# Optimization experiments

Measured on AMD Instinct MI355X. Metric: run time of the kernel, lower is better.

The kernel has to match this reference:

```python
import jax, jax.numpy as jnp
import numpy as np

G, S, M = 4, 2048, 1024   # groups (batch), tokens per group, emb dim
E, H, K = 8, 4096, 2      # experts, mlp dim, top-k
CAP = int(K * S / E * 1.25)  # expert capacity = 640
AUX_COEF, Z_COEF = 0.01, 0.001


def setup_inputs() -> dict:
    key = jax.random.key(0)
    k1, k2, k3, k4, k5 = jax.random.split(key, 5)
    return {
        "inputs": jax.random.normal(k1, (G, S, M), jnp.float32),
        "paddings": jnp.zeros((G, S), jnp.float32),  # 1.0 = padded token
        "router_w": jax.random.normal(k2, (M, E), jnp.float32) / np.sqrt(M),
        "wi_gate": jax.random.normal(k3, (E, M, H), jnp.float32) / np.sqrt(M),
        "wi_0": jax.random.normal(k4, (E, M, H), jnp.float32) / np.sqrt(M),
        "wo": jax.random.normal(k5, (E, H, M), jnp.float32) / np.sqrt(H),
    }


def reference(inputs, paddings, router_w, wi_gate, wi_0, wo):
    # Router
    logits = jnp.einsum('gsm,me->gse', inputs, router_w)          # [G,S,E]
    probs = jax.nn.softmax(logits, axis=-1)
    top_p, top_i = jax.lax.top_k(probs, K)                        # [G,S,K]

    nonpad = 1.0 - paddings                                       # [G,S]
    exp_mask = jax.nn.one_hot(top_i, E, dtype=jnp.float32)        # [G,S,K,E]
    exp_mask = exp_mask * nonpad[:, :, None, None]

    # Position in expert (capacity-limited), priority by token order then k slot
    mask_flat = exp_mask.reshape(G, S * K, E)
    pos = jnp.cumsum(mask_flat, axis=1) * mask_flat               # 1-indexed where assigned
    keep = mask_flat * (pos <= CAP)
    pos_oh = jax.nn.one_hot((pos - 1.0).astype(jnp.int32), CAP, dtype=jnp.float32)  # [G,SK,E,CAP]
    dispatch_k = (keep[..., None] * pos_oh).reshape(G, S, K, E, CAP)
    dispatch = dispatch_k.sum(axis=2)                             # [G,S,E,CAP]
    combine = jnp.einsum('gsk,gskec->gsec', top_p, dispatch_k)    # [G,S,E,CAP]

    # Dispatch -> gated expert FFN -> combine
    expert_in = jnp.einsum('gsec,gsm->egcm', dispatch, inputs)    # [E,G,CAP,M]
    h = jax.nn.silu(jnp.einsum('egcm,emh->egch', expert_in, wi_gate)) \
        * jnp.einsum('egcm,emh->egch', expert_in, wi_0)           # [E,G,CAP,H]
    expert_out = jnp.einsum('egch,ehm->egcm', h, wo)              # [E,G,CAP,M]
    output = jnp.einsum('gsec,egcm->gsm', combine, expert_out)    # [G,S,M]

    # Aux losses: load-balancing (Switch style) + router z-loss
    em = jnp.max(jax.nn.one_hot(top_i, E, dtype=jnp.float32), axis=-2)       # [G,S,E]
    lb = jnp.mean(jnp.mean(em, axis=-2) * jnp.mean(probs, axis=-2)) * E * E
    z = jnp.mean(jax.nn.logsumexp(logits, axis=-1) ** 2)
    aux_loss = AUX_COEF * lb + Z_COEF * z
    return output, aux_loss
```

## Files before the change

### kernel.cpp

```cpp
#include <hip/hip_runtime.h>
#include <hip/hip_bf16.h>
#include <math.h>

#define G 4
#define S 2048
#define MDIM 1024
#define E 8
#define HDIM 4096
#define TOPK 2
#define CAP 640
#define GC (G*CAP)

typedef __attribute__((ext_vector_type(8))) short bf16x8;
typedef __attribute__((ext_vector_type(4))) short s16x4;
typedef __attribute__((ext_vector_type(4))) float f32x4;
typedef unsigned int u32;
typedef unsigned short u16;

#define MFMA16(a,b,c) __builtin_amdgcn_mfma_f32_16x16x32_bf16(a,b,c,0,0,0)

__device__ __forceinline__ u16 f2bf(float f) {
    union { float f; u32 u; } v; v.f = f;
    u32 r = v.u + 0x7fffu + ((v.u >> 16) & 1u);
    return (u16)(r >> 16);
}

__device__ __forceinline__ void gload16(const char* gp, char* lp) {
    __builtin_amdgcn_global_load_lds((const __attribute__((address_space(1))) u32*)gp,
                                     (__attribute__((address_space(3))) u32*)lp,
                                     16, 0, 0);
}

__device__ __forceinline__ int swzb(int r) { return ((r >> 1) & 3) << 4; }

__global__ __launch_bounds__(256) void transpose_cvt(const float* __restrict__ in,
                                                     u16* __restrict__ out, int R, int C) {
    int e = blockIdx.z;
    const float* ine = in + (size_t)e * R * C;
    u16* oute = out + (size_t)e * R * C;
    __shared__ float tile[64][68];
    int t = threadIdx.x;
    int x0 = blockIdx.x * 64, y0 = blockIdx.y * 64;
    int lx = (t & 15) * 4, ly = t >> 4;
    #pragma unroll
    for (int i = 0; i < 4; ++i) {
        f32x4 v = *(const f32x4*)(ine + (size_t)(y0 + ly + i * 16) * C + x0 + lx);
        *(f32x4*)&tile[ly + i * 16][lx] = v;
    }
    __syncthreads();
    int rr0 = (t & 15) * 4, cb = t >> 4;
    #pragma unroll
    for (int p = 0; p < 4; ++p) {
        int cc = cb + p * 16;
        s16x4 pk;
        #pragma unroll
        for (int j = 0; j < 4; ++j) pk[j] = (short)f2bf(tile[rr0 + j][cc]);
        *(s16x4*)(oute + (size_t)(x0 + cc) * R + y0 + rr0) = pk;
    }
}

__global__ __launch_bounds__(256) void router_kernel(const float* __restrict__ inp,
                                                     const float* __restrict__ rw,
                                                     int* __restrict__ top_i,
                                                     float* __restrict__ top_p,
                                                     float* __restrict__ partials) {
    int wid = threadIdx.x >> 6, lane = threadIdx.x & 63;
    int tok = blockIdx.x * 4 + wid;
    const float* x = inp + (size_t)tok * MDIM;
    float acc[E] = {0.f,0.f,0.f,0.f,0.f,0.f,0.f,0.f};
    #pragma unroll
    for (int rep = 0; rep < 4; ++rep) {
        int m0 = rep * 256 + lane * 4;
        f32x4 xv = *(const f32x4*)(x + m0);
        #pragma unroll
        for (int j = 0; j < 4; ++j) {
            const float* r = rw + (size_t)(m0 + j) * E;
            float xj = xv[j];
            #pragma unroll
            for (int e = 0; e < E; ++e) acc[e] += xj * r[e];
        }
    }
    #pragma unroll
    for (int e = 0; e < E; ++e)
        #pragma unroll
        for (int off = 32; off; off >>= 1) acc[e] += __shfl_down(acc[e], off);

    __shared__ float part[4][17];
    if (lane == 0) {
        float mx = acc[0];
        #pragma unroll
        for (int e = 1; e < E; ++e) mx = fmaxf(mx, acc[e]);
        float p[E], sum = 0.f;
        #pragma unroll
        for (int e = 0; e < E; ++e) { p[e] = expf(acc[e] - mx); sum += p[e]; }
        float inv = 1.f / sum;
        #pragma unroll
        for (int e = 0; e < E; ++e) p[e] *= inv;
        float lse = logf(sum) + mx;
        int i0 = 0;
        #pragma unroll
        for (int e = 1; e < E; ++e) if (acc[e] > acc[i0]) i0 = e;
        int i1 = (i0 == 0) ? 1 : 0;
        #pragma unroll
        for (int e = 0; e < E; ++e) if (e != i0 && acc[e] > acc[i1]) i1 = e;
        top_i[tok*2+0] = i0; top_i[tok*2+1] = i1;
        top_p[tok*2+0] = p[i0]; top_p[tok*2+1] = p[i1];
        #pragma unroll
        for (int e = 0; e < E; ++e) { part[wid][e] = p[e]; part[wid][8+e] = 0.f; }
        part[wid][8+i0] = 1.f; part[wid][8+i1] = 1.f;
        part[wid][16] = lse * lse;
    }
    __syncthreads();
    if (threadIdx.x < 17) {
        float v = part[0][threadIdx.x] + part[1][threadIdx.x] +
                  part[2][threadIdx.x] + part[3][threadIdx.x];
        partials[(size_t)blockIdx.x * 17 + threadIdx.x] = v;
    }
}

__global__ __launch_bounds__(256) void reduce_partials(const float* __restrict__ partials,
                                                       float* __restrict__ sums) {
    int g = blockIdx.x, t = threadIdx.x;
    float loc[17];
    #pragma unroll
    for (int c = 0; c < 17; ++c) loc[c] = 0.f;
    for (int r = t; r < 1024; r += 256) {
        const float* pr = partials + ((size_t)g * 1024 + r) * 17;
        #pragma unroll
        for (int c = 0; c < 17; ++c) loc[c] += pr[c];
    }
    __shared__ float red[256];
    for (int c = 0; c < 17; ++c) {
        red[t] = loc[c]; __syncthreads();
        for (int off = 128; off; off >>= 1) {
            if (t < off) red[t] += red[t + off];
            __syncthreads();
        }
        if (t == 0) sums[g * 17 + c] = red[0];
        __syncthreads();
    }
}

__global__ void aux_final(const float* __restrict__ sums, float* __restrict__ out) {
    float lb = 0.f, z = 0.f;
    for (int g = 0; g < G; ++g) {
        for (int e = 0; e < E; ++e)
            lb += (sums[g*17 + 8 + e] / (float)S) * (sums[g*17 + e] / (float)S);
        z += sums[g*17 + 16];
    }
    lb = lb / (float)(G * E) * (float)(E * E);
    z /= (float)(G * S);
    out[(size_t)G * S * MDIM] = 0.01f * lb + 0.001f * z;
}

__global__ __launch_bounds__(256) void scan_kernel(const int* __restrict__ top_i,
                                                   const float* __restrict__ pad,
                                                   int* __restrict__ slot_token,
                                                   int* __restrict__ token_c) {
    int b = blockIdx.x; int g = b >> 3, e = b & 7;
    int t = threadIdx.x;
    __shared__ int sums[256];
    int base = t * 16;
    int run = 0; unsigned mask16 = 0; int loc[16];
    #pragma unroll
    for (int j = 0; j < 16; ++j) {
        int i = base + j; int s = i >> 1, k = i & 1;
        int ex = top_i[((size_t)(g * S + s)) * 2 + k];
        int m = (ex == e) && (pad[g * S + s] == 0.f);
        run += m; loc[j] = run; mask16 |= ((unsigned)m << j);
    }
    sums[t] = run; __syncthreads();
    for (int off = 1; off < 256; off <<= 1) {
        int v = (t >= off) ? sums[t - off] : 0;
        __syncthreads();
        sums[t] += v;
        __syncthreads();
    }
    int excl = sums[t] - run;
    #pragma unroll
    for (int j = 0; j < 16; ++j) {
        if ((mask16 >> j) & 1u) {
            int pos = excl + loc[j];
            if (pos <= CAP) {
                int i = base + j; int s = i >> 1, k = i & 1;
                slot_token[((size_t)(e * G + g)) * CAP + (pos - 1)] = s;
                token_c[((size_t)(g * S + s)) * 2 + k] = pos - 1;
            }
        }
    }
}

__global__ __launch_bounds__(128) void gather_kernel(const float* __restrict__ inp,
                                                     const int* __restrict__ slot_token,
                                                     u16* __restrict__ X) {
    int row = blockIdx.x;
    int t = threadIdx.x;
    int s = slot_token[row];
    int g = (row % GC) / CAP;
    bf16x8 v;
    if (s >= 0) {
        const float* src = inp + ((size_t)(g * S + s)) * MDIM + t * 8;
        f32x4 a = *(const f32x4*)src;
        f32x4 b = *(const f32x4*)(src + 4);
        #pragma unroll
        for (int j = 0; j < 4; ++j) { v[j] = (short)f2bf(a[j]); v[4+j] = (short)f2bf(b[j]); }
    } else {
        #pragma unroll
        for (int j = 0; j < 8; ++j) v[j] = 0;
    }
    *(bf16x8*)(X + (size_t)row * MDIM + t * 8) = v;
}

__global__ __launch_bounds__(512, 1) void gemm_ffn12_v5(
        const u16* __restrict__ Xb, const u16* __restrict__ WgT,
        const u16* __restrict__ W0T, u16* __restrict__ Hb) {
    extern __shared__ char smem[];
    const int NK = MDIM / 32;
    int bid = blockIdx.x;
    int swz = (bid & 7) * 320 + (bid >> 3);
    int mt = swz % 10, nt = (swz / 10) & 31, e = swz / 320;
    const char* A  = (const char*)(Xb  + (size_t)e * GC * MDIM   + (size_t)mt * 256 * MDIM);
    const char* Bg = (const char*)(WgT + (size_t)e * HDIM * MDIM + (size_t)nt * 128 * MDIM);
    const char* B0 = (const char*)(W0T + (size_t)e * HDIM * MDIM + (size_t)nt * 128 * MDIM);
    int tid = threadIdx.x, w = tid >> 6, l = tid & 63;
    int wm = w >> 2, wn = w & 3;
    int rl = l >> 2, cch = (l & 3) * 16;
    int fr = l & 15, fg = l >> 4;
    int lswz = ((fr >> 1) & 3) << 4;

    int rA0 = (0 * 8 + w) * 16 + rl, rA1 = (1 * 8 + w) * 16 + rl, rB = w * 16 + rl;
    const char* gA0 = A  + (size_t)rA0 * MDIM * 2 + (cch ^ swzb(rA0));
    const char* gA1 = A  + (size_t)rA1 * MDIM * 2 + (cch ^ swzb(rA1));
    const char* gBg = Bg + (size_t)rB  * MDIM * 2 + (cch ^ swzb(rB));
    const char* gB0 = B0 + (size_t)rB  * MDIM * 2 + (cch ^ swzb(rB));
    int baseA = (wm * 128 + fr) * 64 + ((fg * 16) ^ lswz);
    int baseB = (wn * 32  + fr) * 64 + ((fg * 16) ^ lswz);

    f32x4 ag[8][2], ao[8][2];
    #pragma unroll
    for (int i = 0; i < 8; ++i) {
        ag[i][0] = (f32x4){0,0,0,0}; ag[i][1] = (f32x4){0,0,0,0};
        ao[i][0] = (f32x4){0,0,0,0}; ao[i][1] = (f32x4){0,0,0,0};
    }

    auto stage = [&](int tt) {
        int kk = tt * 64, b = tt & 3;
        gload16(gA0 + kk, smem + b * 16384 + (0 * 8 + w) * 1024);
        gload16(gA1 + kk, smem + b * 16384 + (1 * 8 + w) * 1024);
        gload16(gBg + kk, smem + 65536 + b * 8192 + w * 1024);
        gload16(gB0 + kk, smem + 98304 + b * 8192 + w * 1024);
    };

    bf16x8 afL0[4], afL1[4];

    stage(0); stage(1);
    asm volatile("s_waitcnt vmcnt(4)" ::: "memory");
    __builtin_amdgcn_s_barrier();
    __builtin_amdgcn_sched_barrier(0);
    {
        const char* p0 = smem + baseA;
        #pragma unroll
        for (int i = 0; i < 4; ++i) afL0[i] = *(const bf16x8*)(p0 + i * 1024);
    }

    auto body = [&](int t, bf16x8 (&loC)[4], bf16x8 (&loN)[4]) {
        if (t + 2 < NK) {
            stage(t + 2);
            asm volatile("s_waitcnt vmcnt(4)" ::: "memory");
        } else {
            asm volatile("s_waitcnt vmcnt(0)" ::: "memory");
        }
        __builtin_amdgcn_s_barrier();
        __builtin_amdgcn_sched_barrier(0);
        const char* pG = smem + 65536 + (t & 3) * 8192 + baseB;
        const char* pO = smem + 98304 + (t & 3) * 8192 + baseB;
        bf16x8 bgf[2], bof[2], hi[4];
        bgf[0] = *(const bf16x8*)(pG);  bgf[1] = *(const bf16x8*)(pG + 1024);
        bof[0] = *(const bf16x8*)(pO);  bof[1] = *(const bf16x8*)(pO + 1024);
        const char* bufA = smem + (t & 3) * 16384 + baseA;
        #pragma unroll
        for (int i = 0; i < 4; ++i) hi[i] = *(const bf16x8*)(bufA + (4 + i) * 1024);
        if (t + 1 < NK) {
            const char* bufN = smem + ((t + 1) & 3) * 16384 + baseA;
            #pragma unroll
            for (int i = 0; i < 4; ++i) loN[i] = *(const bf16x8*)(bufN + i * 1024);
        }
        __builtin_amdgcn_s_setprio(1);
        #pragma unroll
        for (int fm = 0; fm < 4; ++fm)
            #pragma unroll
            for (int fn = 0; fn < 2; ++fn) {
                ag[fm][fn] = MFMA16(bgf[fn], loC[fm], ag[fm][fn]);
                ao[fm][fn] = MFMA16(bof[fn], loC[fm], ao[fm][fn]);
            }
        #pragma unroll
        for (int fm = 0; fm < 4; ++fm)
            #pragma unroll
            for (int fn = 0; fn < 2; ++fn) {
                ag[4+fm][fn] = MFMA16(bgf[fn], hi[fm], ag[4+fm][fn]);
                ao[4+fm][fn] = MFMA16(bof[fn], hi[fm], ao[4+fm][fn]);
            }
        __builtin_amdgcn_s_setprio(0);
    };

    #pragma unroll 1
    for (int t = 0; t < NK; t += 2) {
        body(t, afL0, afL1);
        body(t + 1, afL1, afL0);
    }

    u16* He = Hb + (size_t)e * GC * HDIM;
    int row0 = mt * 256 + wm * 128 + fr;
    int col0 = nt * 128 + wn * 32 + fg * 4;
    #pragma unroll
    for (int fm = 0; fm < 8; ++fm)
        #pragma unroll
        for (int fn = 0; fn < 2; ++fn) {
            s16x4 pk;
            #pragma unroll
            for (int r = 0; r < 4; ++r) {
                float gv = ag[fm][fn][r], ov = ao[fm][fn][r];
                float hv = gv / (1.f + __expf(-gv)) * ov;
                pk[r] = (short)f2bf(hv);
            }
            *(s16x4*)(He + (size_t)(row0 + fm * 16) * HDIM + col0 + fn * 16) = pk;
        }
}

__global__ __launch_bounds__(512, 1) void gemm_out_v4(
        const u16* __restrict__ Hb, const u16* __restrict__ WoT,
        float* __restrict__ EO) {
    extern __shared__ char smem[];
    const int NK = HDIM / 32;
    int bid = blockIdx.x;
    int swz = (bid & 7) * 80 + (bid >> 3);
    int nt = swz & 3, mt = (swz / 4) % 20, e = swz / 80;
    const char* A = (const char*)(Hb  + (size_t)e * GC * HDIM   + (size_t)mt * 128 * HDIM);
    const char* B = (const char*)(WoT + (size_t)e * MDIM * HDIM + (size_t)nt * 256 * HDIM);
    int tid = threadIdx.x, w = tid >> 6, l = tid & 63;
    int wm = w >> 2, wn = w & 3;
    int rl = l >> 2, cch = (l & 3) * 16;
    int fr = l & 15, fg = l >> 4;
    int lswz = ((fr >> 1) & 3) << 4;

    int rA = w * 16 + rl, rB0 = (0 * 8 + w) * 16 + rl, rB1 = (1 * 8 + w) * 16 + rl;
    const char* gA  = A + (size_t)rA  * HDIM * 2 + (cch ^ swzb(rA));
    const char* gBa = B + (size_t)rB0 * HDIM * 2 + (cch ^ swzb(rB0));
    const char* gBb = B + (size_t)rB1 * HDIM * 2 + (cch ^ swzb(rB1));
    int baseA = (wm * 64 + fr) * 64 + ((fg * 16) ^ lswz);
    int baseB = (wn * 64 + fr) * 64 + ((fg * 16) ^ lswz);

    f32x4 acc[4][4];
    #pragma unroll
    for (int i = 0; i < 4; ++i)
        #pragma unroll
        for (int j = 0; j < 4; ++j) acc[i][j] = (f32x4){0,0,0,0};

    auto stage = [&](int tt) {
        int kk = tt * 64, b = tt & 3;
        gload16(gA  + kk, smem + b * 8192 + w * 1024);
        gload16(gBa + kk, smem + 32768 + b * 16384 + (0 * 8 + w) * 1024);
        gload16(gBb + kk, smem + 32768 + b * 16384 + (1 * 8 + w) * 1024);
    };

    bf16x8 afA[4], bfA[4], afB[4], bfB[4];

    stage(0); stage(1);
    asm volatile("s_waitcnt vmcnt(3)" ::: "memory");
    __builtin_amdgcn_s_barrier();
    __builtin_amdgcn_sched_barrier(0);
    {
        const char* pA = smem + baseA;
        const char* pB = smem + 32768 + baseB;
        #pragma unroll
        for (int i = 0; i < 4; ++i) {
            afA[i] = *(const bf16x8*)(pA + i * 1024);
            bfA[i] = *(const bf16x8*)(pB + i * 1024);
        }
    }

    auto body = [&](int t, bf16x8 (&afc)[4], bf16x8 (&bfc)[4],
                    bf16x8 (&afn)[4], bf16x8 (&bfn)[4]) {
        if (t + 2 < NK) {
            stage(t + 2);
            asm volatile("s_waitcnt vmcnt(3)" ::: "memory");
        } else {
            asm volatile("s_waitcnt vmcnt(0)" ::: "memory");
        }
        __builtin_amdgcn_s_barrier();
        __builtin_amdgcn_sched_barrier(0);
        if (t + 1 < NK) {
            const char* pA = smem + ((t + 1) & 3) * 8192 + baseA;
            const char* pB = smem + 32768 + ((t + 1) & 3) * 16384 + baseB;
            #pragma unroll
            for (int i = 0; i < 4; ++i) {
                afn[i] = *(const bf16x8*)(pA + i * 1024);
                bfn[i] = *(const bf16x8*)(pB + i * 1024);
            }
        }
        __builtin_amdgcn_s_setprio(1);
        #pragma unroll
        for (int fm = 0; fm < 4; ++fm)
            #pragma unroll
            for (int fn = 0; fn < 4; ++fn)
                acc[fm][fn] = MFMA16(bfc[fn], afc[fm], acc[fm][fn]);
        __builtin_amdgcn_s_setprio(0);
    };

    #pragma unroll 1
    for (int t = 0; t < NK; t += 2) {
        body(t, afA, bfA, afB, bfB);
        body(t + 1, afB, bfB, afA, bfA);
    }

    float* Ee = EO + (size_t)e * GC * MDIM;
    int row0 = mt * 128 + wm * 64 + fr;
    int col0 = nt * 256 + wn * 64 + fg * 4;
    #pragma unroll
    for (int fm = 0; fm < 4; ++fm)
        #pragma unroll
        for (int fn = 0; fn < 4; ++fn)
            *(f32x4*)(Ee + (size_t)(row0 + fm * 16) * MDIM + col0 + fn * 16) = acc[fm][fn];
}

__global__ __launch_bounds__(256) void combine_kernel(const float* __restrict__ EO,
                                                      const int* __restrict__ top_i,
                                                      const float* __restrict__ top_p,
                                                      const int* __restrict__ token_c,
                                                      float* __restrict__ out) {
    int tok = blockIdx.x, t = threadIdx.x;
    int g = tok >> 11;
    f32x4 acc = {0.f, 0.f, 0.f, 0.f};
    #pragma unroll
    for (int k = 0; k < 2; ++k) {
        int c = token_c[tok * 2 + k];
        if (c >= 0) {
            int e = top_i[tok * 2 + k];
            float p = top_p[tok * 2 + k];
            const float* src = EO + ((size_t)e * GC + g * CAP + c) * MDIM + t * 4;
            f32x4 v = *(const f32x4*)src;
            #pragma unroll
            for (int j = 0; j < 4; ++j) acc[j] += p * v[j];
        }
    }
    *(f32x4*)(out + (size_t)tok * MDIM + t * 4) = acc;
}

extern "C" void kernel_launch(void* const* d_in, const int* in_sizes, int n_in,
                              void* d_out, int out_size, void* d_ws, size_t ws_size,
                              hipStream_t stream) {
    (void)in_sizes; (void)n_in; (void)out_size; (void)ws_size;
    const float* inputs   = (const float*)d_in[0];
    const float* paddings = (const float*)d_in[1];
    const float* router_w = (const float*)d_in[2];
    const float* wi_gate  = (const float*)d_in[3];
    const float* wi_0     = (const float*)d_in[4];
    const float* wo       = (const float*)d_in[5];
    float* out = (float*)d_out;

    char* p = (char*)d_ws;
    u16* WgT = (u16*)p; p += (size_t)E * HDIM * MDIM * 2;
    u16* W0T = (u16*)p; p += (size_t)E * HDIM * MDIM * 2;
    u16* WoT = (u16*)p; p += (size_t)E * HDIM * MDIM * 2;
    u16* Xb  = (u16*)p; p += (size_t)E * GC * MDIM * 2;
    u16* Hb  = (u16*)p; p += (size_t)E * GC * HDIM * 2;
    float* EO = (float*)p; p += (size_t)E * GC * MDIM * 4;
    int*   top_i = (int*)p;   p += (size_t)G * S * TOPK * 4;
    float* top_p = (float*)p; p += (size_t)G * S * TOPK * 4;
    int*   token_c = (int*)p; p += (size_t)G * S * TOPK * 4;
    int*   slot_token = (int*)p; p += (size_t)E * G * CAP * 4;
    float* partials = (float*)p; p += (size_t)4096 * 17 * 4;
    float* sums = (float*)p; p += 4 * 17 * 4;

    hipMemsetAsync(token_c, 0xFF, (size_t)G * S * TOPK * 4, stream);
    hipMemsetAsync(slot_token, 0xFF, (size_t)E * G * CAP * 4, stream);

    hipFuncSetAttribute((const void*)gemm_ffn12_v5,
                        hipFuncAttributeMaxDynamicSharedMemorySize, 131072);
    hipFuncSetAttribute((const void*)gemm_out_v4,
                        hipFuncAttributeMaxDynamicSharedMemorySize, 98304);

    transpose_cvt<<<dim3(HDIM/64, MDIM/64, E), 256, 0, stream>>>(wi_gate, WgT, MDIM, HDIM);
    transpose_cvt<<<dim3(HDIM/64, MDIM/64, E), 256, 0, stream>>>(wi_0,   W0T, MDIM, HDIM);
    transpose_cvt<<<dim3(MDIM/64, HDIM/64, E), 256, 0, stream>>>(wo,     WoT, HDIM, MDIM);

    router_kernel<<<G * S / 4, 256, 0, stream>>>(inputs, router_w, top_i, top_p, partials);
    reduce_partials<<<G, 256, 0, stream>>>(partials, sums);
    scan_kernel<<<G * E, 256, 0, stream>>>(top_i, paddings, slot_token, token_c);
    gather_kernel<<<E * GC, 128, 0, stream>>>(inputs, slot_token, Xb);
    gemm_ffn12_v5<<<2560, 512, 131072, stream>>>(Xb, WgT, W0T, Hb);
    gemm_out_v4<<<640, 512, 98304, stream>>>(Hb, WoT, EO);
    combine_kernel<<<G * S, 256, 0, stream>>>(EO, top_i, top_p, token_c, out);
    aux_final<<<1, 1, 0, stream>>>(sums, out);
}
```

Baseline: 796.8 us.

## Restructure expert GEMMs to 4-wave blocks with 2 blocks per CU

Both expert GEMM kernels move from 8-wave, single-block-per-CU designs with 4-stage LDS pipelines and register prefetch to 4-wave blocks with a simple double-buffered LDS pipeline and 48KB shared memory, allowing two blocks per CU. The FFN12 kernel shrinks its M tile from 256 to 128 rows, doubling its grid. The output GEMM gives each wave a larger 64x128 accumulator tile. The intent is better latency hiding through occupancy rather than deep software pipelining. The cost is a full vmcnt(0) wait plus barrier every K step and larger per-wave register footprints.

```diff
diff --git a/kernel.cpp b/kernel.cpp
--- a/kernel.cpp
+++ b/kernel.cpp
@@ -211,111 +211,85 @@
     *(bf16x8*)(X + (size_t)row * MDIM + t * 8) = v;
 }
 
-__global__ __launch_bounds__(512, 1) void gemm_ffn12_v5(
+__global__ __launch_bounds__(256, 2) void gemm_ffn12_v6(
         const u16* __restrict__ Xb, const u16* __restrict__ WgT,
         const u16* __restrict__ W0T, u16* __restrict__ Hb) {
     extern __shared__ char smem[];
     const int NK = MDIM / 32;
     int bid = blockIdx.x;
-    int swz = (bid & 7) * 320 + (bid >> 3);
-    int mt = swz % 10, nt = (swz / 10) & 31, e = swz / 320;
-    const char* A  = (const char*)(Xb  + (size_t)e * GC * MDIM   + (size_t)mt * 256 * MDIM);
+    int swz = (bid & 7) * 640 + (bid >> 3);
+    int mt = swz % 20, nt = (swz / 20) % 32, e = swz / 640;
+    const char* A  = (const char*)(Xb  + (size_t)e * GC * MDIM   + (size_t)mt * 128 * MDIM);
     const char* Bg = (const char*)(WgT + (size_t)e * HDIM * MDIM + (size_t)nt * 128 * MDIM);
     const char* B0 = (const char*)(W0T + (size_t)e * HDIM * MDIM + (size_t)nt * 128 * MDIM);
     int tid = threadIdx.x, w = tid >> 6, l = tid & 63;
-    int wm = w >> 2, wn = w & 3;
+    int wm = w >> 1, wn = w & 1;
     int rl = l >> 2, cch = (l & 3) * 16;
     int fr = l & 15, fg = l >> 4;
     int lswz = ((fr >> 1) & 3) << 4;
 
-    int rA0 = (0 * 8 + w) * 16 + rl, rA1 = (1 * 8 + w) * 16 + rl, rB = w * 16 + rl;
-    const char* gA0 = A  + (size_t)rA0 * MDIM * 2 + (cch ^ swzb(rA0));
-    const char* gA1 = A  + (size_t)rA1 * MDIM * 2 + (cch ^ swzb(rA1));
-    const char* gBg = Bg + (size_t)rB  * MDIM * 2 + (cch ^ swzb(rB));
-    const char* gB0 = B0 + (size_t)rB  * MDIM * 2 + (cch ^ swzb(rB));
-    int baseA = (wm * 128 + fr) * 64 + ((fg * 16) ^ lswz);
-    int baseB = (wn * 32  + fr) * 64 + ((fg * 16) ^ lswz);
-
-    f32x4 ag[8][2], ao[8][2];
-    #pragma unroll
-    for (int i = 0; i < 8; ++i) {
-        ag[i][0] = (f32x4){0,0,0,0}; ag[i][1] = (f32x4){0,0,0,0};
-        ao[i][0] = (f32x4){0,0,0,0}; ao[i][1] = (f32x4){0,0,0,0};
-    }
+    int r0 = 0 * 64 + w * 16 + rl, r1 = 1 * 64 + w * 16 + rl;
+    const char* gA0 = A  + (size_t)r0 * MDIM * 2 + (cch ^ swzb(r0));
+    const char* gA1 = A  + (size_t)r1 * MDIM * 2 + (cch ^ swzb(r1));
+    const char* gG0 = Bg + (size_t)r0 * MDIM * 2 + (cch ^ swzb(r0));
+    const char* gG1 = Bg + (size_t)r1 * MDIM * 2 + (cch ^ swzb(r1));
+    const char* gO0 = B0 + (size_t)r0 * MDIM * 2 + (cch ^ swzb(r0));
+    const char* gO1 = B0 + (size_t)r1 * MDIM * 2 + (cch ^ swzb(r1));
+    int baseA = (wm * 64 + fr) * 64 + ((fg * 16) ^ lswz);
+    int baseB = (wn * 64 + fr) * 64 + ((fg * 16) ^ lswz);
+
+    f32x4 ag[4][4], ao[4][4];
+    #pragma unroll
+    for (int i = 0; i < 4; ++i)
+        #pragma unroll
+        for (int j = 0; j < 4; ++j) { ag[i][j] = (f32x4){0,0,0,0}; ao[i][j] = (f32x4){0,0,0,0}; }
 
     auto stage = [&](int tt) {
-        int kk = tt * 64, b = tt & 3;
-        gload16(gA0 + kk, smem + b * 16384 + (0 * 8 + w) * 1024);
-        gload16(gA1 + kk, smem + b * 16384 + (1 * 8 + w) * 1024);
-        gload16(gBg + kk, smem + 65536 + b * 8192 + w * 1024);
-        gload16(gB0 + kk, smem + 98304 + b * 8192 + w * 1024);
+        int kk = tt * 64;
+        char* dst = smem + (tt & 1) * 24576;
+        gload16(gA0 + kk, dst + 0 * 4096 + w * 1024);
+        gload16(gA1 + kk, dst + 1 * 4096 + w * 1024);
+        gload16(gG0 + kk, dst + 8192 + 0 * 4096 + w * 1024);
+        gload16(gG1 + kk, dst + 8192 + 1 * 4096 + w * 1024);
+        gload16(gO0 + kk, dst + 16384 + 0 * 4096 + w * 1024);
+        gload16(gO1 + kk, dst + 16384 + 1 * 4096 + w * 1024);
     };
 
-    bf16x8 afL0[4], afL1[4];
-
-    stage(0); stage(1);
-    asm volatile("s_waitcnt vmcnt(4)" ::: "memory");
+    stage(0);
+    asm volatile("s_waitcnt vmcnt(0)" ::: "memory");
     __builtin_amdgcn_s_barrier();
-    __builtin_amdgcn_sched_barrier(0);
-    {
-        const char* p0 = smem + baseA;
-        #pragma unroll
-        for (int i = 0; i < 4; ++i) afL0[i] = *(const bf16x8*)(p0 + i * 1024);
-    }
-
-    auto body = [&](int t, bf16x8 (&loC)[4], bf16x8 (&loN)[4]) {
-        if (t + 2 < NK) {
-            stage(t + 2);
-            asm volatile("s_waitcnt vmcnt(4)" ::: "memory");
-        } else {
-            asm volatile("s_waitcnt vmcnt(0)" ::: "memory");
-        }
-        __builtin_amdgcn_s_barrier();
-        __builtin_amdgcn_sched_barrier(0);
-        const char* pG = smem + 65536 + (t & 3) * 8192 + baseB;
-        const char* pO = smem + 98304 + (t & 3) * 8192 + baseB;
-        bf16x8 bgf[2], bof[2], hi[4];
-        bgf[0] = *(const bf16x8*)(pG);  bgf[1] = *(const bf16x8*)(pG + 1024);
-        bof[0] = *(const bf16x8*)(pO);  bof[1] = *(const bf16x8*)(pO + 1024);
-        const char* bufA = smem + (t & 3) * 16384 + baseA;
-        #pragma unroll
-        for (int i = 0; i < 4; ++i) hi[i] = *(const bf16x8*)(bufA + (4 + i) * 1024);
-        if (t + 1 < NK) {
-            const char* bufN = smem + ((t + 1) & 3) * 16384 + baseA;
-            #pragma unroll
-            for (int i = 0; i < 4; ++i) loN[i] = *(const bf16x8*)(bufN + i * 1024);
-        }
+
+    #pragma unroll 1
+    for (int t = 0; t < NK; ++t) {
+        if (t + 1 < NK) stage(t + 1);
+        const char* bufc = smem + (t & 1) * 24576;
+        bf16x8 af[4], bg_[4], bo_[4];
+        #pragma unroll
+        for (int fm = 0; fm < 4; ++fm) af[fm]  = *(const bf16x8*)(bufc + baseA + fm * 1024);
+        #pragma unroll
+        for (int fn = 0; fn < 4; ++fn) bg_[fn] = *(const bf16x8*)(bufc + 8192  + baseB + fn * 1024);
+        #pragma unroll
+        for (int fn = 0; fn < 4; ++fn) bo_[fn] = *(const bf16x8*)(bufc + 16384 + baseB + fn * 1024);
         __builtin_amdgcn_s_setprio(1);
         #pragma unroll
         for (int fm = 0; fm < 4; ++fm)
             #pragma unroll
-            for (int fn = 0; fn < 2; ++fn) {
-                ag[fm][fn] = MFMA16(bgf[fn], loC[fm], ag[fm][fn]);
-                ao[fm][fn] = MFMA16(bof[fn], loC[fm], ao[fm][fn]);
-            }
-        #pragma unroll
-        for (int fm = 0; fm < 4; ++fm)
-            #pragma unroll
-            for (int fn = 0; fn < 2; ++fn) {
-                ag[4+fm][fn] = MFMA16(bgf[fn], hi[fm], ag[4+fm][fn]);
-                ao[4+fm][fn] = MFMA16(bof[fn], hi[fm], ao[4+fm][fn]);
+            for (int fn = 0; fn < 4; ++fn) {
+                ag[fm][fn] = MFMA16(bg_[fn], af[fm], ag[fm][fn]);
+                ao[fm][fn] = MFMA16(bo_[fn], af[fm], ao[fm][fn]);
             }
         __builtin_amdgcn_s_setprio(0);
-    };
-
-    #pragma unroll 1
-    for (int t = 0; t < NK; t += 2) {
-        body(t, afL0, afL1);
-        body(t + 1, afL1, afL0);
+        asm volatile("s_waitcnt vmcnt(0)" ::: "memory");
+        __builtin_amdgcn_s_barrier();
     }
 
     u16* He = Hb + (size_t)e * GC * HDIM;
-    int row0 = mt * 256 + wm * 128 + fr;
-    int col0 = nt * 128 + wn * 32 + fg * 4;
-    #pragma unroll
-    for (int fm = 0; fm < 8; ++fm)
-        #pragma unroll
-        for (int fn = 0; fn < 2; ++fn) {
+    int row0 = mt * 128 + wm * 64 + fr;
+    int col0 = nt * 128 + wn * 64 + fg * 4;
+    #pragma unroll
+    for (int fm = 0; fm < 4; ++fm)
+        #pragma unroll
+        for (int fn = 0; fn < 4; ++fn) {
             s16x4 pk;
             #pragma unroll
             for (int r = 0; r < 4; ++r) {
@@ -327,99 +301,81 @@
         }
 }
 
-__global__ __launch_bounds__(512, 1) void gemm_out_v4(
+__global__ __launch_bounds__(256, 2) void gemm_out_v6(
         const u16* __restrict__ Hb, const u16* __restrict__ WoT,
         float* __restrict__ EO) {
     extern __shared__ char smem[];
     const int NK = HDIM / 32;
     int bid = blockIdx.x;
     int swz = (bid & 7) * 80 + (bid >> 3);
-    int nt = swz & 3, mt = (swz / 4) % 20, e = swz / 80;
+    int mt = swz % 20, nt = (swz / 20) & 3, e = swz / 80;
     const char* A = (const char*)(Hb  + (size_t)e * GC * HDIM   + (size_t)mt * 128 * HDIM);
     const char* B = (const char*)(WoT + (size_t)e * MDIM * HDIM + (size_t)nt * 256 * HDIM);
     int tid = threadIdx.x, w = tid >> 6, l = tid & 63;
-    int wm = w >> 2, wn = w & 3;
+    int wm = w >> 1, wn = w & 1;
     int rl = l >> 2, cch = (l & 3) * 16;
     int fr = l & 15, fg = l >> 4;
     int lswz = ((fr >> 1) & 3) << 4;
 
-    int rA = w * 16 + rl, rB0 = (0 * 8 + w) * 16 + rl, rB1 = (1 * 8 + w) * 16 + rl;
-    const char* gA  = A + (size_t)rA  * HDIM * 2 + (cch ^ swzb(rA));
-    const char* gBa = B + (size_t)rB0 * HDIM * 2 + (cch ^ swzb(rB0));
-    const char* gBb = B + (size_t)rB1 * HDIM * 2 + (cch ^ swzb(rB1));
-    int baseA = (wm * 64 + fr) * 64 + ((fg * 16) ^ lswz);
-    int baseB = (wn * 64 + fr) * 64 + ((fg * 16) ^ lswz);
-
-    f32x4 acc[4][4];
+    int r0 = 0 * 64 + w * 16 + rl, r1 = 1 * 64 + w * 16 + rl;
+    int r2 = 2 * 64 + w * 16 + rl, r3 = 3 * 64 + w * 16 + rl;
+    const char* gA0 = A + (size_t)r0 * HDIM * 2 + (cch ^ swzb(r0));
+    const char* gA1 = A + (size_t)r1 * HDIM * 2 + (cch ^ swzb(r1));
+    const char* gB0 = B + (size_t)r0 * HDIM * 2 + (cch ^ swzb(r0));
+    const char* gB1 = B + (size_t)r1 * HDIM * 2 + (cch ^ swzb(r1));
+    const char* gB2 = B + (size_t)r2 * HDIM * 2 + (cch ^ swzb(r2));
+    const char* gB3 = B + (size_t)r3 * HDIM * 2 + (cch ^ swzb(r3));
+    int baseA = (wm * 64  + fr) * 64 + ((fg * 16) ^ lswz);
+    int baseB = (wn * 128 + fr) * 64 + ((fg * 16) ^ lswz);
+
+    f32x4 acc[4][8];
     #pragma unroll
     for (int i = 0; i < 4; ++i)
         #pragma unroll
-        for (int j = 0; j < 4; ++j) acc[i][j] = (f32x4){0,0,0,0};
+        for (int j = 0; j < 8; ++j) acc[i][j] = (f32x4){0,0,0,0};
 
     auto stage = [&](int tt) {
-        int kk = tt * 64, b = tt & 3;
-        gload16(gA  + kk, smem + b * 8192 + w * 1024);
-        gload16(gBa + kk, smem + 32768 + b * 16384 + (0 * 8 + w) * 1024);
-        gload16(gBb + kk, smem + 32768 + b * 16384 + (1 * 8 + w) * 1024);
+        int kk = tt * 64;
+        char* dst = smem + (tt & 1) * 24576;
+        gload16(gA0 + kk, dst + 0 * 4096 + w * 1024);
+        gload16(gA1 + kk, dst + 1 * 4096 + w * 1024);
+        gload16(gB0 + kk, dst + 8192 + 0 * 4096 + w * 1024);
+        gload16(gB1 + kk, dst + 8192 + 1 * 4096 + w * 1024);
+        gload16(gB2 + kk, dst + 8192 + 2 * 4096 + w * 1024);
+        gload16(gB3 + kk, dst + 8192 + 3 * 4096 + w * 1024);
     };
 
-    bf16x8 afA[4], bfA[4], afB[4], bfB[4];
-
-    stage(0); stage(1);
-    asm volatile("s_waitcnt vmcnt(3)" ::: "memory");
+    stage(0);
+    asm volatile("s_waitcnt vmcnt(0)" ::: "memory");
     __builtin_amdgcn_s_barrier();
-    __builtin_amdgcn_sched_barrier(0);
-    {
-        const char* pA = smem + baseA;
-        const char* pB = smem + 32768 + baseB;
-        #pragma unroll
-        for (int i = 0; i < 4; ++i) {
-            afA[i] = *(const bf16x8*)(pA + i * 1024);
-            bfA[i] = *(const bf16x8*)(pB + i * 1024);
-        }
-    }
-
-    auto body = [&](int t, bf16x8 (&afc)[4], bf16x8 (&bfc)[4],
-                    bf16x8 (&afn)[4], bf16x8 (&bfn)[4]) {
-        if (t + 2 < NK) {
-            stage(t + 2);
-            asm volatile("s_waitcnt vmcnt(3)" ::: "memory");
-        } else {
-            asm volatile("s_waitcnt vmcnt(0)" ::: "memory");
-        }
-        __builtin_amdgcn_s_barrier();
-        __builtin_amdgcn_sched_barrier(0);
-        if (t + 1 < NK) {
-            const char* pA = smem + ((t + 1) & 3) * 8192 + baseA;
-            const char* pB = smem + 32768 + ((t + 1) & 3) * 16384 + baseB;
-            #pragma unroll
-            for (int i = 0; i < 4; ++i) {
-                afn[i] = *(const bf16x8*)(pA + i * 1024);
-                bfn[i] = *(const bf16x8*)(pB + i * 1024);
-            }
-        }
+
+    #pragma unroll 1
+    for (int t = 0; t < NK; ++t) {
+        if (t + 1 < NK) stage(t + 1);
+        const char* bufc = smem + (t & 1) * 24576;
+        bf16x8 af[4], bf[8];
+        #pragma unroll
+        for (int fm = 0; fm < 4; ++fm) af[fm] = *(const bf16x8*)(bufc + baseA + fm * 1024);
+        #pragma unroll
+        for (int fn = 0; fn < 8; ++fn) bf[fn] = *(const bf16x8*)(bufc + 8192 + baseB + fn * 1024);
         __builtin_amdgcn_s_setprio(1);
         #pragma unroll
         for (int fm = 0; fm < 4; ++fm)
             #pragma unroll
-            for (int fn = 0; fn < 4; ++fn)
-                acc[fm][fn] = MFMA16(bfc[fn], afc[fm], acc[fm][fn]);
+            for (int fn = 0; fn < 8; ++fn)
+                acc[fm][fn] = MFMA16(bf[fn], af[fm], acc[fm][fn]);
         __builtin_amdgcn_s_setprio(0);
-    };
-
-    #pragma unroll 1
-    for (int t = 0; t < NK; t += 2) {
-        body(t, afA, bfA, afB, bfB);
-        body(t + 1, afB, bfB, afA, bfA);
+        asm volatile("s_waitcnt vmcnt(0)" ::: "memory");
+        __builtin_amdgcn_s_barrier();
     }
 
     float* Ee = EO + (size_t)e * GC * MDIM;
     int row0 = mt * 128 + wm * 64 + fr;
-    int col0 = nt * 256 + wn * 64 + fg * 4;
+    int col0 = nt * 256 + wn * 128 + fg * 4;
     #pragma unroll
     for (int fm = 0; fm < 4; ++fm)
         #pragma unroll
-        for (int fn = 0; fn < 4; ++fn)
+        for (int fn = 0; fn < 8; ++fn)
             *(f32x4*)(Ee + (size_t)(row0 + fm * 16) * MDIM + col0 + fn * 16) = acc[fm][fn];
 }
 
@@ -475,10 +431,10 @@
     hipMemsetAsync(token_c, 0xFF, (size_t)G * S * TOPK * 4, stream);
     hipMemsetAsync(slot_token, 0xFF, (size_t)E * G * CAP * 4, stream);
 
-    hipFuncSetAttribute((const void*)gemm_ffn12_v5,
-                        hipFuncAttributeMaxDynamicSharedMemorySize, 131072);
-    hipFuncSetAttribute((const void*)gemm_out_v4,
-                        hipFuncAttributeMaxDynamicSharedMemorySize, 98304);
+    hipFuncSetAttribute((const void*)gemm_ffn12_v6,
+                        hipFuncAttributeMaxDynamicSharedMemorySize, 49152);
+    hipFuncSetAttribute((const void*)gemm_out_v6,
+                        hipFuncAttributeMaxDynamicSharedMemorySize, 49152);
 
     transpose_cvt<<<dim3(HDIM/64, MDIM/64, E), 256, 0, stream>>>(wi_gate, WgT, MDIM, HDIM);
     transpose_cvt<<<dim3(HDIM/64, MDIM/64, E), 256, 0, stream>>>(wi_0,   W0T, MDIM, HDIM);
@@ -488,8 +444,8 @@
     reduce_partials<<<G, 256, 0, stream>>>(partials, sums);
     scan_kernel<<<G * E, 256, 0, stream>>>(top_i, paddings, slot_token, token_c);
     gather_kernel<<<E * GC, 128, 0, stream>>>(inputs, slot_token, Xb);
-    gemm_ffn12_v5<<<2560, 512, 131072, stream>>>(Xb, WgT, W0T, Hb);
-    gemm_out_v4<<<640, 512, 98304, stream>>>(Hb, WoT, EO);
+    gemm_ffn12_v6<<<5120, 256, 49152, stream>>>(Xb, WgT, W0T, Hb);
+    gemm_out_v6<<<640, 256, 49152, stream>>>(Hb, WoT, EO);
     combine_kernel<<<G * S, 256, 0, stream>>>(EO, top_i, top_p, token_c, out);
     aux_final<<<1, 1, 0, stream>>>(sums, out);
 }
```

Result: no change. 802.8 us (+0.7%).

## Replace register-prefetch pipelines with barrier-phased LDS loads in both expert GEMMs

Applied to the files above, without the earlier changes.

Both expert GEMM kernels drop the double-buffered register prefetch of the next k-step's LDS fragments. Each iteration now loads the current fragments and synchronizes with extra block barriers and lgkmcnt(0) waits, so all waves run their MFMA phases in lockstep. The FFN12 kernel also splits each k-step into two half-phases (low and high A rows) with a barrier between them. This lowers register pressure and aligns the waves, but it adds barriers and exposes LDS latency that the prefetch used to hide.

```diff
diff --git a/kernel.cpp b/kernel.cpp
--- a/kernel.cpp
+++ b/kernel.cpp
@@ -18,6 +18,9 @@
 typedef unsigned short u16;
 
 #define MFMA16(a,b,c) __builtin_amdgcn_mfma_f32_16x16x32_bf16(a,b,c,0,0,0)
+#define SB0() __builtin_amdgcn_sched_barrier(0)
+#define BAR() __builtin_amdgcn_s_barrier()
+#define LGKM0() asm volatile("s_waitcnt lgkmcnt(0)" ::: "memory")
 
 __device__ __forceinline__ u16 f2bf(float f) {
     union { float f; u32 u; } v; v.f = f;
@@ -211,7 +214,7 @@
     *(bf16x8*)(X + (size_t)row * MDIM + t * 8) = v;
 }
 
-__global__ __launch_bounds__(512, 1) void gemm_ffn12_v5(
+__global__ __launch_bounds__(512, 1) void gemm_ffn12_v7(
         const u16* __restrict__ Xb, const u16* __restrict__ WgT,
         const u16* __restrict__ W0T, u16* __restrict__ Hb) {
     extern __shared__ char smem[];
@@ -251,62 +254,52 @@
         gload16(gB0 + kk, smem + 98304 + b * 8192 + w * 1024);
     };
 
-    bf16x8 afL0[4], afL1[4];
-
     stage(0); stage(1);
     asm volatile("s_waitcnt vmcnt(4)" ::: "memory");
-    __builtin_amdgcn_s_barrier();
-    __builtin_amdgcn_sched_barrier(0);
-    {
-        const char* p0 = smem + baseA;
-        #pragma unroll
-        for (int i = 0; i < 4; ++i) afL0[i] = *(const bf16x8*)(p0 + i * 1024);
-    }
-
-    auto body = [&](int t, bf16x8 (&loC)[4], bf16x8 (&loN)[4]) {
-        if (t + 2 < NK) {
-            stage(t + 2);
-            asm volatile("s_waitcnt vmcnt(4)" ::: "memory");
-        } else {
-            asm volatile("s_waitcnt vmcnt(0)" ::: "memory");
-        }
-        __builtin_amdgcn_s_barrier();
-        __builtin_amdgcn_sched_barrier(0);
+    BAR();
+
+    #pragma unroll 1
+    for (int t = 0; t < NK; ++t) {
+        if (t + 2 < NK) stage(t + 2);
+        const char* bufA = smem + (t & 3) * 16384 + baseA;
         const char* pG = smem + 65536 + (t & 3) * 8192 + baseB;
         const char* pO = smem + 98304 + (t & 3) * 8192 + baseB;
-        bf16x8 bgf[2], bof[2], hi[4];
+        bf16x8 bgf[2], bof[2], af[4];
         bgf[0] = *(const bf16x8*)(pG);  bgf[1] = *(const bf16x8*)(pG + 1024);
         bof[0] = *(const bf16x8*)(pO);  bof[1] = *(const bf16x8*)(pO + 1024);
-        const char* bufA = smem + (t & 3) * 16384 + baseA;
-        #pragma unroll
-        for (int i = 0; i < 4; ++i) hi[i] = *(const bf16x8*)(bufA + (4 + i) * 1024);
-        if (t + 1 < NK) {
-            const char* bufN = smem + ((t + 1) & 3) * 16384 + baseA;
-            #pragma unroll
-            for (int i = 0; i < 4; ++i) loN[i] = *(const bf16x8*)(bufN + i * 1024);
-        }
+        #pragma unroll
+        for (int i = 0; i < 4; ++i) af[i] = *(const bf16x8*)(bufA + i * 1024);
+        SB0();
+        BAR();
+        LGKM0(); SB0();
         __builtin_amdgcn_s_setprio(1);
         #pragma unroll
         for (int fm = 0; fm < 4; ++fm)
             #pragma unroll
             for (int fn = 0; fn < 2; ++fn) {
-                ag[fm][fn] = MFMA16(bgf[fn], loC[fm], ag[fm][fn]);
-                ao[fm][fn] = MFMA16(bof[fn], loC[fm], ao[fm][fn]);
-            }
-        #pragma unroll
-        for (int fm = 0; fm < 4; ++fm)
-            #pragma unroll
-            for (int fn = 0; fn < 2; ++fn) {
-                ag[4+fm][fn] = MFMA16(bgf[fn], hi[fm], ag[4+fm][fn]);
-                ao[4+fm][fn] = MFMA16(bof[fn], hi[fm], ao[4+fm][fn]);
+                ag[fm][fn] = MFMA16(bgf[fn], af[fm], ag[fm][fn]);
+                ao[fm][fn] = MFMA16(bof[fn], af[fm], ao[fm][fn]);
             }
         __builtin_amdgcn_s_setprio(0);
-    };
-
-    #pragma unroll 1
-    for (int t = 0; t < NK; t += 2) {
-        body(t, afL0, afL1);
-        body(t + 1, afL1, afL0);
+        BAR();
+        bf16x8 ah[4];
+        #pragma unroll
+        for (int i = 0; i < 4; ++i) ah[i] = *(const bf16x8*)(bufA + (4 + i) * 1024);
+        SB0();
+        if (t + 2 < NK) { asm volatile("s_waitcnt vmcnt(4)" ::: "memory"); }
+        else            { asm volatile("s_waitcnt vmcnt(0)" ::: "memory"); }
+        BAR();
+        LGKM0(); SB0();
+        __builtin_amdgcn_s_setprio(1);
+        #pragma unroll
+        for (int fm = 0; fm < 4; ++fm)
+            #pragma unroll
+            for (int fn = 0; fn < 2; ++fn) {
+                ag[4+fm][fn] = MFMA16(bgf[fn], ah[fm], ag[4+fm][fn]);
+                ao[4+fm][fn] = MFMA16(bof[fn], ah[fm], ao[4+fm][fn]);
+            }
+        __builtin_amdgcn_s_setprio(0);
+        BAR();
     }
 
     u16* He = Hb + (size_t)e * GC * HDIM;
@@ -327,7 +320,7 @@
         }
 }
 
-__global__ __launch_bounds__(512, 1) void gemm_out_v4(
+__global__ __launch_bounds__(512, 1) void gemm_out_v7(
         const u16* __restrict__ Hb, const u16* __restrict__ WoT,
         float* __restrict__ EO) {
     extern __shared__ char smem[];
@@ -363,54 +356,34 @@
         gload16(gBb + kk, smem + 32768 + b * 16384 + (1 * 8 + w) * 1024);
     };
 
-    bf16x8 afA[4], bfA[4], afB[4], bfB[4];
-
     stage(0); stage(1);
     asm volatile("s_waitcnt vmcnt(3)" ::: "memory");
-    __builtin_amdgcn_s_barrier();
-    __builtin_amdgcn_sched_barrier(0);
-    {
-        const char* pA = smem + baseA;
-        const char* pB = smem + 32768 + baseB;
+    BAR();
+
+    #pragma unroll 1
+    for (int t = 0; t < NK; ++t) {
+        if (t + 2 < NK) stage(t + 2);
+        const char* pA = smem + (t & 3) * 8192 + baseA;
+        const char* pB = smem + 32768 + (t & 3) * 16384 + baseB;
+        bf16x8 af[4], bf[4];
         #pragma unroll
         for (int i = 0; i < 4; ++i) {
-            afA[i] = *(const bf16x8*)(pA + i * 1024);
-            bfA[i] = *(const bf16x8*)(pB + i * 1024);
-        }
-    }
-
-    auto body = [&](int t, bf16x8 (&afc)[4], bf16x8 (&bfc)[4],
-                    bf16x8 (&afn)[4], bf16x8 (&bfn)[4]) {
-        if (t + 2 < NK) {
-            stage(t + 2);
-            asm volatile("s_waitcnt vmcnt(3)" ::: "memory");
-        } else {
-            asm volatile("s_waitcnt vmcnt(0)" ::: "memory");
-        }
-        __builtin_amdgcn_s_barrier();
-        __builtin_amdgcn_sched_barrier(0);
-        if (t + 1 < NK) {
-            const char* pA = smem + ((t + 1) & 3) * 8192 + baseA;
-            const char* pB = smem + 32768 + ((t + 1) & 3) * 16384 + baseB;
-            #pragma unroll
-            for (int i = 0; i < 4; ++i) {
-                afn[i] = *(const bf16x8*)(pA + i * 1024);
-                bfn[i] = *(const bf16x8*)(pB + i * 1024);
-            }
-        }
+            af[i] = *(const bf16x8*)(pA + i * 1024);
+            bf[i] = *(const bf16x8*)(pB + i * 1024);
+        }
+        SB0();
+        if (t + 2 < NK) { asm volatile("s_waitcnt vmcnt(3)" ::: "memory"); }
+        else            { asm volatile("s_waitcnt vmcnt(0)" ::: "memory"); }
+        BAR();
+        LGKM0(); SB0();
         __builtin_amdgcn_s_setprio(1);
         #pragma unroll
         for (int fm = 0; fm < 4; ++fm)
             #pragma unroll
             for (int fn = 0; fn < 4; ++fn)
-                acc[fm][fn] = MFMA16(bfc[fn], afc[fm], acc[fm][fn]);
+                acc[fm][fn] = MFMA16(bf[fn], af[fm], acc[fm][fn]);
         __builtin_amdgcn_s_setprio(0);
-    };
-
-    #pragma unroll 1
-    for (int t = 0; t < NK; t += 2) {
-        body(t, afA, bfA, afB, bfB);
-        body(t + 1, afB, bfB, afA, bfA);
+        BAR();
     }
 
     float* Ee = EO + (size_t)e * GC * MDIM;
@@ -475,9 +448,9 @@
     hipMemsetAsync(token_c, 0xFF, (size_t)G * S * TOPK * 4, stream);
     hipMemsetAsync(slot_token, 0xFF, (size_t)E * G * CAP * 4, stream);
 
-    hipFuncSetAttribute((const void*)gemm_ffn12_v5,
+    hipFuncSetAttribute((const void*)gemm_ffn12_v7,
                         hipFuncAttributeMaxDynamicSharedMemorySize, 131072);
-    hipFuncSetAttribute((const void*)gemm_out_v4,
+    hipFuncSetAttribute((const void*)gemm_out_v7,
                         hipFuncAttributeMaxDynamicSharedMemorySize, 98304);
 
     transpose_cvt<<<dim3(HDIM/64, MDIM/64, E), 256, 0, stream>>>(wi_gate, WgT, MDIM, HDIM);
@@ -488,8 +461,8 @@
     reduce_partials<<<G, 256, 0, stream>>>(partials, sums);
     scan_kernel<<<G * E, 256, 0, stream>>>(top_i, paddings, slot_token, token_c);
     gather_kernel<<<E * GC, 128, 0, stream>>>(inputs, slot_token, Xb);
-    gemm_ffn12_v5<<<2560, 512, 131072, stream>>>(Xb, WgT, W0T, Hb);
-    gemm_out_v4<<<640, 512, 98304, stream>>>(Hb, WoT, EO);
+    gemm_ffn12_v7<<<2560, 512, 131072, stream>>>(Xb, WgT, W0T, Hb);
+    gemm_out_v7<<<640, 512, 98304, stream>>>(Hb, WoT, EO);
     combine_kernel<<<G * S, 256, 0, stream>>>(EO, top_i, top_p, token_c, out);
     aux_final<<<1, 1, 0, stream>>>(sums, out);
 }
```

Measured after the change: 817.8 us. +2.6%, slower.
